# Optimization experiments

Measured on AMD Instinct MI355X. Metric: run time of the kernel, lower is better.

## Reference

```python
import jax, jax.numpy as jnp
import numpy as np

K = 128      # scratch_keys_dim
NP = 3       # n_pointers
P = 200      # program_dim
STEPS = 3    # max_program_steps


def _positional_encoding(max_len=50, d=K):
    pos = np.arange(max_len, dtype=np.float32)[:, None]
    div = np.exp(np.arange(0, d, 2, dtype=np.float32) * (-np.log(10000.0) / d))
    pe = np.zeros((max_len, d), dtype=np.float32)
    pe[:, 0::2] = np.sin(pos * div)
    pe[:, 1::2] = np.cos(pos * div)
    return jnp.asarray(pe)


def setup_inputs() -> dict:
    B, I, L, Vin, Vout = 256, 16, 50, 1000, 512
    H = K * NP
    key = jax.random.key(0)
    ks = jax.random.split(key, 8)
    s = 0.05
    return {
        'instructions': jax.random.randint(ks[0], (I, B), 0, Vin),
        'true_actions': jax.random.randint(ks[1], (L, B), 0, Vout),
        'gate_emb': jax.random.normal(ks[2], (Vin, 2), jnp.float32) * s,
        'program_emb': jax.random.normal(ks[3], (Vin, P), jnp.float32) * s,
        'primitive_emb': jax.random.normal(ks[4], (Vin, Vout), jnp.float32) * s,
        'w_ih': jax.random.normal(ks[5], (3 * H, P), jnp.float32) * s,
        'w_hh': jax.random.normal(ks[6], (3 * H, H), jnp.float32) * s,
        'b_ih': jnp.zeros((3 * H,), jnp.float32),
        'b_hh': jnp.zeros((3 * H,), jnp.float32),
        'scratch_keys': _positional_encoding(),
        'init_value': jnp.zeros((Vout,), jnp.float32).at[0].set(1.0),  # one-hot eos
    }


def _gru_cell(x, h, w_ih, w_hh, b_ih, b_hh):
    # torch.nn.GRUCell math
    gi = x @ w_ih.T + b_ih
    gh = h @ w_hh.T + b_hh
    i_r, i_z, i_n = jnp.split(gi, 3, axis=-1)
    h_r, h_z, h_n = jnp.split(gh, 3, axis=-1)
    r = jax.nn.sigmoid(i_r + h_r)
    z = jax.nn.sigmoid(i_z + h_z)
    n = jnp.tanh(i_n + r * h_n)
    return (1.0 - z) * n + z * h


def reference(instructions, true_actions, gate_emb, program_emb, primitive_emb,
              w_ih, w_hh, b_ih, b_hh, scratch_keys, init_value):
    I, B = instructions.shape
    L = true_actions.shape[0]
    keys = scratch_keys[:L]                                    # [L,K], broadcast over batch
    h0 = jnp.tile(scratch_keys[0], (B, NP))                    # [B,3K] init executor hidden
    v0 = jnp.broadcast_to(init_value, (B, L, init_value.shape[0]))  # [B,L,Vout]

    def outer(carry, word):
        h, vals = carry
        gate = jax.nn.softmax(gate_emb[word], axis=-1)         # [B,2] (softmax gate activation)
        program = program_emb[word]                            # [B,P]
        primitive = primitive_emb[word]                        # [B,Vout]
        for _ in range(STEPS):
            read_ptr = h[:, K:2 * K]                           # [B,K]
            write_ptr = h[:, 2 * K:3 * K]                      # [B,K]
            read_attn = jax.nn.softmax(jnp.einsum('bk,lk->bl', read_ptr, keys), axis=-1)
            read_value = jnp.einsum('bl,blv->bv', read_attn, vals)
            # gate-weighted mix of primitive and read value
            new_value = gate[:, :1] * primitive + gate[:, 1:] * read_value   # [B,Vout]
            write_mask = jax.nn.softmax(jnp.einsum('bk,lk->bl', write_ptr, keys), axis=-1)
            vals = write_mask[:, :, None] * new_value[:, None, :] + (1.0 - write_mask[:, :, None]) * vals
            h = _gru_cell(program, h, w_ih, w_hh, b_ih, b_hh)
        return (h, vals), None

    (h, vals), _ = jax.lax.scan(outer, (h0, v0), instructions)
    actions = jnp.transpose(jax.nn.log_softmax(vals, axis=-1), (0, 2, 1))  # [B,Vout,L]
    return actions, true_actions.T
```

## Files before the change

### kernel.cpp

```cpp
#include <hip/hip_runtime.h>
#include <math.h>

#define KK     128
#define HH     384
#define H3     1152
#define PP     200
#define LL     50
#define VV     512
#define BB     256
#define II     16
#define NSTEPS 3

#define NT     640
#define KPW    132
#define VP2    258

#define GH4G   12
#define GIG    13
#define WQ4H_UI (GH4G * 3 * 384 * 4)
#define WQI_UI  (GIG  * 3 * 384 * 4)

__device__ __forceinline__ int dot4(unsigned a, unsigned b, int c) {
    return __builtin_amdgcn_sdot4((int)a, (int)b, c, false);
}
__device__ __forceinline__ int dot8(unsigned a, unsigned b, int c) {
    return __builtin_amdgcn_sdot8((int)a, (int)b, c, false);
}
__device__ __forceinline__ float rcpf(float x) { return __builtin_amdgcn_rcpf(x); }
__device__ __forceinline__ float sigm(float x) { return rcpf(1.f + __expf(-x)); }
__device__ __forceinline__ float tanh_fast(float x) {
    float xc = fminf(fmaxf(x, -15.f), 15.f);
    float t = __expf(2.f * xc);
    return 1.f - 2.f * rcpf(t + 1.f);
}
__device__ __forceinline__ int q8(float x, float sc) {
    int q = (int)rintf(x * sc);
    return q < -127 ? -127 : (q > 127 ? 127 : q);
}
__device__ __forceinline__ int q4(float x, float sc) {
    int q = (int)rintf(x * sc);
    return q < -7 ? -7 : (q > 7 ? 7 : q);
}

__global__ void wmax_reduce(const float* __restrict__ w_hh,
                            const float* __restrict__ w_ih,
                            const float* __restrict__ prog_emb,
                            unsigned* __restrict__ scales)
{
    int idx = blockIdx.x * 256 + threadIdx.x;
    int stride = gridDim.x * 256;
    float mh = 0.f, mi = 0.f, mp = 0.f;
    for (int i = idx; i < HH * H3; i += stride) mh = fmaxf(mh, fabsf(w_hh[i]));
    for (int i = idx; i < PP * H3; i += stride) mi = fmaxf(mi, fabsf(w_ih[i]));
    for (int i = idx; i < 1000 * PP; i += stride) mp = fmaxf(mp, fabsf(prog_emb[i]));
    #pragma unroll
    for (int mm = 32; mm >= 1; mm >>= 1) {
        mh = fmaxf(mh, __shfl_xor(mh, mm, 64));
        mi = fmaxf(mi, __shfl_xor(mi, mm, 64));
        mp = fmaxf(mp, __shfl_xor(mp, mm, 64));
    }
    if ((threadIdx.x & 63) == 0) {
        atomicMax(scales,     __float_as_uint(mh));
        atomicMax(scales + 1, __float_as_uint(mi));
        atomicMax(scales + 2, __float_as_uint(mp));
    }
}

__global__ void pack_weights(const float* __restrict__ w_hh,
                             const float* __restrict__ w_ih,
                             const unsigned* __restrict__ scales,
                             unsigned* __restrict__ wq)
{
    int idx = blockIdx.x * 256 + threadIdx.x;
    if (idx < WQ4H_UI) {
        const float sc = 7.f * rcpf(fmaxf(__uint_as_float(scales[0]), 1e-20f));
        int u4 = idx >> 2, m = idx & 3;
        int g = u4 / (3 * 384);
        int r = u4 - g * (3 * 384);
        int s = r / 384, t = r - s * 384;
        int j = t + 384 * s, k = 32 * g + 8 * m;
        const float* wr = w_hh + (long)j * HH + k;
        unsigned pw = 0;
        #pragma unroll
        for (int e = 0; e < 8; ++e) pw |= ((unsigned)(q4(wr[e], sc) & 0xF)) << (4 * e);
        wq[idx] = pw;
    } else if (idx < WQ4H_UI + WQI_UI) {
        const float sc = 127.f * rcpf(fmaxf(__uint_as_float(scales[1]), 1e-20f));
        int q = idx - WQ4H_UI;
        int u4 = q >> 2, m = q & 3;
        int g = u4 / (3 * 384);
        int r = u4 - g * (3 * 384);
        int s = r / 384, t = r - s * 384;
        int j = t + 384 * s, k = 16 * g + 4 * m;
        unsigned pw = 0;
        #pragma unroll
        for (int e = 0; e < 4; ++e) {
            float w = (k + e < PP) ? w_ih[(long)j * PP + k + e] : 0.f;
            pw |= ((unsigned)(q8(w, sc) & 255)) << (8 * e);
        }
        wq[WQ4H_UI + u4 * 4 + m] = pw;
    }
}

struct __align__(16) Smem {
    float2 vals[LL * VP2];
    float  keys[LL * KPW];
    float  h[HH]            __attribute__((aligned(16)));
    unsigned hq4[HH / 8]    __attribute__((aligned(16)));
    unsigned progq[56]      __attribute__((aligned(16)));
    float  rl[52], wl[52];
    float  raw[4][52], wmw[4][52];
    float  rowoff[52];
    float  partial[4 * 52];
};

__global__ __launch_bounds__(NT)
void symop_main(const int* __restrict__ instr,
                const float* __restrict__ gate_emb,
                const float* __restrict__ program_emb,
                const float* __restrict__ primitive_emb,
                const uint4* __restrict__ wqhh,
                const uint4* __restrict__ wqih,
                const unsigned* __restrict__ scales,
                const float* __restrict__ b_ih,
                const float* __restrict__ b_hh,
                const float* __restrict__ keys_g,
                const float* __restrict__ init_value,
                float* __restrict__ out)
{
    __shared__ Smem sm;

    const int tid  = threadIdx.x;
    const int lane = tid & 63;
    const int wid  = tid >> 6;
    const int b    = blockIdx.x;

    const float maxH = fmaxf(__uint_as_float(scales[0]), 1e-20f);
    const float maxI = fmaxf(__uint_as_float(scales[1]), 1e-20f);
    const float maxP = fmaxf(__uint_as_float(scales[2]), 1e-20f);
    const float ghs = maxH * (1.f / 49.f);
    const float gis = maxI * maxP * (1.f / 16129.f);
    const float psc = 127.f * rcpf(maxP);

    for (int idx = tid; idx < LL * KK; idx += NT) {
        int l = idx >> 7, k = idx & 127;
        sm.keys[l * KPW + k] = keys_g[idx];
    }
    float hcur = 0.f;
    if (tid < HH) {
        hcur = keys_g[tid & 127];
        sm.h[tid] = hcur;
    }
    if (tid < HH / 8) {
        unsigned pw = 0;
        #pragma unroll
        for (int e = 0; e < 8; ++e) {
            int q = (int)rintf(keys_g[(8 * tid + e) & 127] * 7.f);
            pw |= ((unsigned)(q & 0xF)) << (4 * e);
        }
        sm.hq4[tid] = pw;
    }
    for (int idx = tid; idx < LL * 256; idx += NT) {
        int l = idx >> 8, c = idx & 255;
        sm.vals[l * VP2 + c] = *(const float2*)(init_value + 2 * c);
    }
    if (tid >= 512 && tid < 512 + 52) {
        int qt = tid - 512;
        int w0 = instr[b];
        const float* pg = program_emb + (long)w0 * PP;
        unsigned pw = 0;
        #pragma unroll
        for (int e = 0; e < 4; ++e) {
            int k = 4 * qt + e;
            float v = (k < PP) ? pg[k] : 0.f;
            pw |= ((unsigned)(q8(v, psc) & 255)) << (8 * e);
        }
        sm.progq[qt] = pw;
    }
    __syncthreads();

    float bh0 = 0, bh1 = 0, bh2 = 0, bi0 = 0, bi1 = 0, bi2 = 0;
    if (tid < HH) {
        bh0 = b_hh[tid]; bh1 = b_hh[tid + HH]; bh2 = b_hh[tid + 2 * HH];
        bi0 = b_ih[tid]; bi1 = b_ih[tid + HH]; bi2 = b_ih[tid + 2 * HH];
    }
    float gic0 = 0, gic1 = 0, gic2 = 0;
    int   gn0 = 0, gn1 = 0, gn2 = 0;

    if (tid < HH) {
        int ia0 = 0, ia1 = 0, ia2 = 0;
        const uint4* wp = wqih + tid;
        #pragma unroll 2
        for (int g = 0; g < GIG; ++g) {
            uint4 w0 = wp[(g * 3 + 0) * 384];
            uint4 w1 = wp[(g * 3 + 1) * 384];
            uint4 w2 = wp[(g * 3 + 2) * 384];
            uint4 hp = *(const uint4*)(sm.progq + 4 * g);
            ia0 = dot4(w0.x, hp.x, ia0); ia0 = dot4(w0.y, hp.y, ia0);
            ia0 = dot4(w0.z, hp.z, ia0); ia0 = dot4(w0.w, hp.w, ia0);
            ia1 = dot4(w1.x, hp.x, ia1); ia1 = dot4(w1.y, hp.y, ia1);
            ia1 = dot4(w1.z, hp.z, ia1); ia1 = dot4(w1.w, hp.w, ia1);
            ia2 = dot4(w2.x, hp.x, ia2); ia2 = dot4(w2.y, hp.y, ia2);
            ia2 = dot4(w2.z, hp.z, ia2); ia2 = dot4(w2.w, hp.w, ia2);
        }
        gic0 = bi0 + (float)ia0 * gis;
        gic1 = bi1 + (float)ia1 * gis;
        gic2 = bi2 + (float)ia2 * gis;
    } else if (tid < HH + 2 * LL) {
        int dd = tid - HH;
        int l = (dd < LL) ? dd : dd - LL;
        const float* p  = (dd < LL) ? (sm.h + KK) : (sm.h + 2 * KK);
        const float* kr = sm.keys + l * KPW;
        float acc = 0.f;
        #pragma unroll 8
        for (int k = 0; k < KK; ++k) acc = fmaf(p[k], kr[k], acc);
        if (dd < LL) sm.rl[l] = acc; else sm.wl[l] = acc;
    }
    __syncthreads();

    for (int i = 0; i < II; ++i) {
        const int word = instr[i * BB + b];
        for (int t = 0; t < NSTEPS; ++t) {
            if (tid < HH) {
                int ia0 = 0, ia1 = 0, ia2 = 0;
                const uint4* wp = wqhh + tid;
                #pragma unroll 2
                for (int g = 0; g < GH4G; ++g) {
                    uint4 w0 = wp[(g * 3 + 0) * 384];
                    uint4 w1 = wp[(g * 3 + 1) * 384];
                    uint4 w2 = wp[(g * 3 + 2) * 384];
                    uint4 hp = *(const uint4*)(sm.hq4 + 4 * g);
                    ia0 = dot8(w0.x, hp.x, ia0); ia0 = dot8(w0.y, hp.y, ia0);
                    ia0 = dot8(w0.z, hp.z, ia0); ia0 = dot8(w0.w, hp.w, ia0);
                    ia1 = dot8(w1.x, hp.x, ia1); ia1 = dot8(w1.y, hp.y, ia1);
                    ia1 = dot8(w1.z, hp.z, ia1); ia1 = dot8(w1.w, hp.w, ia1);
                    ia2 = dot8(w2.x, hp.x, ia2); ia2 = dot8(w2.y, hp.y, ia2);
                    ia2 = dot8(w2.z, hp.z, ia2); ia2 = dot8(w2.w, hp.w, ia2);
                }
                const float gh0 = bh0 + (float)ia0 * ghs;
                const float gh1 = bh1 + (float)ia1 * ghs;
                const float gh2 = bh2 + (float)ia2 * ghs;

                if (i + 1 < II) {
                    const uint4* wi = wqih + tid;
                    if (t == 1) {
                        gn0 = 0; gn1 = 0; gn2 = 0;
                        #pragma unroll 2
                        for (int g = 0; g < 7; ++g) {
                            uint4 w0 = wi[(g * 3 + 0) * 384];
                            uint4 w1 = wi[(g * 3 + 1) * 384];
                            uint4 w2 = wi[(g * 3 + 2) * 384];
                            uint4 hp = *(const uint4*)(sm.progq + 4 * g);
                            gn0 = dot4(w0.x, hp.x, gn0); gn0 = dot4(w0.y, hp.y, gn0);
                            gn0 = dot4(w0.z, hp.z, gn0); gn0 = dot4(w0.w, hp.w, gn0);
                            gn1 = dot4(w1.x, hp.x, gn1); gn1 = dot4(w1.y, hp.y, gn1);
                            gn1 = dot4(w1.z, hp.z, gn1); gn1 = dot4(w1.w, hp.w, gn1);
                            gn2 = dot4(w2.x, hp.x, gn2); gn2 = dot4(w2.y, hp.y, gn2);
                            gn2 = dot4(w2.z, hp.z, gn2); gn2 = dot4(w2.w, hp.w, gn2);
                        }
                    } else if (t == 2) {
                        #pragma unroll 2
                        for (int g = 7; g < GIG; ++g) {
                            uint4 w0 = wi[(g * 3 + 0) * 384];
                            uint4 w1 = wi[(g * 3 + 1) * 384];
                            uint4 w2 = wi[(g * 3 + 2) * 384];
                            uint4 hp = *(const uint4*)(sm.progq + 4 * g);
                            gn0 = dot4(w0.x, hp.x, gn0); gn0 = dot4(w0.y, hp.y, gn0);
                            gn0 = dot4(w0.z, hp.z, gn0); gn0 = dot4(w0.w, hp.w, gn0);
                            gn1 = dot4(w1.x, hp.x, gn1); gn1 = dot4(w1.y, hp.y, gn1);
                            gn1 = dot4(w1.z, hp.z, gn1); gn1 = dot4(w1.w, hp.w, gn1);
                            gn2 = dot4(w2.x, hp.x, gn2); gn2 = dot4(w2.y, hp.y, gn2);
                            gn2 = dot4(w2.z, hp.z, gn2); gn2 = dot4(w2.w, hp.w, gn2);
                        }
                    }
                }

                const float r = sigm(gic0 + gh0);
                const float z = sigm(gic1 + gh1);
                const float n = tanh_fast(gic2 + r * gh2);
                const float hn = (1.f - z) * n + z * hcur;
                hcur = hn;
                sm.h[tid] = hn;
                int q = ((int)rintf(hn * 7.f)) & 0xF;
                unsigned u1 = (unsigned)q | ((unsigned)__shfl_down(q, 1, 64) << 4);
                unsigned u2 = u1 | (__shfl_down((int)u1, 2, 64) << 8);
                unsigned u4 = u2 | (__shfl_down((int)u2, 4, 64) << 16);
                if (!(tid & 7)) sm.hq4[tid >> 3] = u4;
                if (t == 2 && i + 1 < II) {
                    gic0 = bi0 + (float)gn0 * gis;
                    gic1 = bi1 + (float)gn1 * gis;
                    gic2 = bi2 + (float)gn2 * gis;
                }
            } else {
                const int w4 = wid - 6;
                float vr = (lane < LL) ? sm.rl[lane] : -1e30f;
                float vw = (lane < LL) ? sm.wl[lane] : -1e30f;
                float mr = vr, mw = vw;
                #pragma unroll
                for (int mm = 32; mm >= 1; mm >>= 1) {
                    mr = fmaxf(mr, __shfl_xor(mr, mm, 64));
                    mw = fmaxf(mw, __shfl_xor(mw, mm, 64));
                }
                float er = (lane < LL) ? __expf(vr - mr) : 0.f;
                float ew = (lane < LL) ? __expf(vw - mw) : 0.f;
                float sr = er, sw = ew;
                #pragma unroll
                for (int mm = 32; mm >= 1; mm >>= 1) {
                    sr += __shfl_xor(sr, mm, 64);
                    sw += __shfl_xor(sw, mm, 64);
                }
                if (lane < LL) {
                    sm.raw[w4][lane] = er * rcpf(sr);
                    sm.wmw[w4][lane] = ew * rcpf(sw);
                }
                const float ge0 = gate_emb[2 * word], ge1 = gate_emb[2 * word + 1];
                const float gmx = fmaxf(ge0, ge1);
                const float e0 = __expf(ge0 - gmx), e1 = __expf(ge1 - gmx);
                const float g0 = e0 * rcpf(e0 + e1), g1 = 1.0f - g0;
                const float* prim = primitive_emb + (long)word * VV;

                const int c = tid - HH;
                float2 pr = *(const float2*)(prim + 2 * c);
                float rv0 = 0.f, rv1 = 0.f;
                #pragma unroll 10
                for (int l = 0; l < LL; ++l) {
                    float2 vv = sm.vals[l * VP2 + c];
                    rv0 = fmaf(sm.raw[w4][l], vv.x, rv0);
                    rv1 = fmaf(sm.raw[w4][l], vv.y, rv1);
                }
                const float nv0 = g0 * pr.x + g1 * rv0;
                const float nv1 = g0 * pr.y + g1 * rv1;
                #pragma unroll 10
                for (int l = 0; l < LL; ++l) {
                    float2 vv = sm.vals[l * VP2 + c];
                    const float w = sm.wmw[w4][l];
                    vv.x = fmaf(w, nv0 - vv.x, vv.x);
                    vv.y = fmaf(w, nv1 - vv.y, vv.y);
                    sm.vals[l * VP2 + c] = vv;
                }
            }
            __syncthreads();

            if (tid < 4 * 2 * LL) {
                const int dot = tid >> 2;
                const int sub = tid & 3;
                const int l   = (dot < LL) ? dot : dot - LL;
                const float* p  = (dot < LL) ? (sm.h + KK) : (sm.h + 2 * KK);
                const float* kr = sm.keys + l * KPW;
                float acc = 0.f;
                #pragma unroll
                for (int kk = 0; kk < KK / 4; ++kk) {
                    int k = sub + 4 * kk;
                    acc = fmaf(p[k], kr[k], acc);
                }
                acc += __shfl_xor(acc, 1, 64);
                acc += __shfl_xor(acc, 2, 64);
                if (sub == 0) {
                    if (dot < LL) sm.rl[l] = acc; else sm.wl[l] = acc;
                }
            } else if (t == 0 && i + 1 < II && tid >= 512 && tid < 512 + 52) {
                int qt = tid - 512;
                int wn = instr[(i + 1) * BB + b];
                const float* pg = program_emb + (long)wn * PP;
                unsigned pw = 0;
                #pragma unroll
                for (int e = 0; e < 4; ++e) {
                    int k = 4 * qt + e;
                    float v = (k < PP) ? pg[k] : 0.f;
                    pw |= ((unsigned)(q8(v, psc) & 255)) << (8 * e);
                }
                sm.progq[qt] = pw;
            }
            __syncthreads();
        }
    }

    if (tid < 256) {
        #pragma unroll 5
        for (int l = 0; l < LL; ++l) {
            float2 vv = sm.vals[l * VP2 + tid];
            float e = __expf(vv.x) + __expf(vv.y);
            #pragma unroll
            for (int mm = 32; mm >= 1; mm >>= 1) e += __shfl_xor(e, mm, 64);
            if (lane == 0) sm.partial[wid * 52 + l] = e;
        }
    }
    __syncthreads();
    if (tid < LL) {
        float s = 0.f;
        #pragma unroll
        for (int w = 0; w < 4; ++w) s += sm.partial[w * 52 + tid];
        sm.rowoff[tid] = logf(s);
    }
    __syncthreads();

    if (tid < 256) {
        float* ob0 = out + (long)b * VV * LL + (long)(2 * tid) * LL;
        float* ob1 = ob0 + LL;
        #pragma unroll 5
        for (int l = 0; l < LL; l += 2) {
            float2 va = sm.vals[l * VP2 + tid];
            float2 vb = sm.vals[(l + 1) * VP2 + tid];
            float o0 = sm.rowoff[l], o1 = sm.rowoff[l + 1];
            *(float2*)(ob0 + l) = make_float2(va.x - o0, vb.x - o1);
            *(float2*)(ob1 + l) = make_float2(va.y - o0, vb.y - o1);
        }
    }
}

__global__ void ta_copy(const int* __restrict__ ta, float* __restrict__ out2)
{
    int idx = blockIdx.x * 256 + threadIdx.x;
    if (idx < BB * LL) {
        int b2 = idx / LL, l = idx % LL;
        out2[idx] = (float)ta[l * BB + b2];
    }
}

extern "C" void kernel_launch(void* const* d_in, const int* in_sizes, int n_in,
                              void* d_out, int out_size, void* d_ws, size_t ws_size,
                              hipStream_t stream)
{
    const int*   instr        = (const int*)  d_in[0];
    const int*   true_actions = (const int*)  d_in[1];
    const float* gate_emb     = (const float*)d_in[2];
    const float* program_emb  = (const float*)d_in[3];
    const float* primitive_emb= (const float*)d_in[4];
    const float* w_ih         = (const float*)d_in[5];
    const float* w_hh         = (const float*)d_in[6];
    const float* b_ih         = (const float*)d_in[7];
    const float* b_hh         = (const float*)d_in[8];
    const float* scratch_keys = (const float*)d_in[9];
    const float* init_value   = (const float*)d_in[10];

    unsigned* scales = (unsigned*)d_ws;
    unsigned* wq     = (unsigned*)d_ws + 4;
    const uint4* wqhh = (const uint4*)wq;
    const uint4* wqih = (const uint4*)(wq + WQ4H_UI);

    hipMemsetAsync(scales, 0, 12, stream);
    wmax_reduce<<<256, 256, 0, stream>>>(w_hh, w_ih, program_emb, scales);
    {
        int total = WQ4H_UI + WQI_UI;
        pack_weights<<<(total + 255) / 256, 256, 0, stream>>>(w_hh, w_ih, scales, wq);
    }

    float* out = (float*)d_out;
    float* out_actions = out;
    float* out_ta      = out + (long)BB * VV * LL;

    symop_main<<<BB, NT, 0, stream>>>(instr, gate_emb, program_emb, primitive_emb,
                                      wqhh, wqih, scales, b_ih, b_hh,
                                      scratch_keys, init_value, out_actions);

    ta_copy<<<(BB * LL + 255) / 256, 256, 0, stream>>>(true_actions, out_ta);
}
```

Baseline: 310.6 us.

## Fuse pointer-key logits into value waves with int8 dot4 and double-buffered hidden

Removes the separate fp32 phase that computed read/write attention logits, and the second barrier per step that followed it. The value-update waves now compute the logits themselves using int8-quantized keys and an int8 copy of the hidden state with sdot4. The quantized hidden state is double-buffered (hq4/hq8 indexed by parity), so the GRU threads can write the next state while the other waves read the current one, leaving one barrier per step. Attention logits now carry int8 quantization error, and each GRU step does extra shuffle/pack work to produce both 4-bit and 8-bit copies of h.

New measurement: 302.7 us (median of 2 runs). 2.6% less time.

```diff
diff --git a/kernel.cpp b/kernel.cpp
--- a/kernel.cpp
+++ b/kernel.cpp
@@ -12,8 +12,8 @@
 #define NSTEPS 3
 
 #define NT     640
-#define KPW    132
 #define VP2    258
+#define KQP    33
 
 #define GH4G   12
 #define GIG    13
@@ -104,11 +104,10 @@
 
 struct __align__(16) Smem {
     float2 vals[LL * VP2];
-    float  keys[LL * KPW];
-    float  h[HH]            __attribute__((aligned(16)));
-    unsigned hq4[HH / 8]    __attribute__((aligned(16)));
+    unsigned keysq[LL * KQP + 16] __attribute__((aligned(16)));
+    unsigned hq4[2][48]     __attribute__((aligned(16)));
+    unsigned hq8[2][96]     __attribute__((aligned(16)));
     unsigned progq[56]      __attribute__((aligned(16)));
-    float  rl[52], wl[52];
     float  raw[4][52], wmw[4][52];
     float  rowoff[52];
     float  partial[4 * 52];
@@ -141,24 +140,35 @@
     const float ghs = maxH * (1.f / 49.f);
     const float gis = maxI * maxP * (1.f / 16129.f);
     const float psc = 127.f * rcpf(maxP);
-
-    for (int idx = tid; idx < LL * KK; idx += NT) {
-        int l = idx >> 7, k = idx & 127;
-        sm.keys[l * KPW + k] = keys_g[idx];
-    }
+    const float lsc = 1.f / 16129.f;
+
     float hcur = 0.f;
-    if (tid < HH) {
-        hcur = keys_g[tid & 127];
-        sm.h[tid] = hcur;
-    }
-    if (tid < HH / 8) {
+    if (tid < HH) hcur = keys_g[tid & 127];
+    for (int idx = tid; idx < LL * 32; idx += NT) {
+        int l = idx >> 5, kk = idx & 31;
+        const float* kr = keys_g + l * KK + 4 * kk;
+        unsigned pw = 0;
+        #pragma unroll
+        for (int e = 0; e < 4; ++e) pw |= ((unsigned)(q8(kr[e], 127.f) & 255)) << (8 * e);
+        sm.keysq[l * KQP + kk] = pw;
+    }
+    if (tid < 96) {
+        unsigned pw = 0;
+        #pragma unroll
+        for (int e = 0; e < 4; ++e) {
+            int q = q8(keys_g[(4 * tid + e) & 127], 127.f);
+            pw |= ((unsigned)(q & 255)) << (8 * e);
+        }
+        sm.hq8[0][tid] = pw;
+    } else if (tid >= 128 && tid < 128 + 48) {
+        int u = tid - 128;
         unsigned pw = 0;
         #pragma unroll
         for (int e = 0; e < 8; ++e) {
-            int q = (int)rintf(keys_g[(8 * tid + e) & 127] * 7.f);
+            int q = q4(keys_g[(8 * u + e) & 127], 7.f);
             pw |= ((unsigned)(q & 0xF)) << (4 * e);
         }
-        sm.hq4[tid] = pw;
+        sm.hq4[0][u] = pw;
     }
     for (int idx = tid; idx < LL * 256; idx += NT) {
         int l = idx >> 8, c = idx & 255;
@@ -206,18 +216,9 @@
         gic0 = bi0 + (float)ia0 * gis;
         gic1 = bi1 + (float)ia1 * gis;
         gic2 = bi2 + (float)ia2 * gis;
-    } else if (tid < HH + 2 * LL) {
-        int dd = tid - HH;
-        int l = (dd < LL) ? dd : dd - LL;
-        const float* p  = (dd < LL) ? (sm.h + KK) : (sm.h + 2 * KK);
-        const float* kr = sm.keys + l * KPW;
-        float acc = 0.f;
-        #pragma unroll 8
-        for (int k = 0; k < KK; ++k) acc = fmaf(p[k], kr[k], acc);
-        if (dd < LL) sm.rl[l] = acc; else sm.wl[l] = acc;
-    }
-    __syncthreads();
-
+    }
+
+    int par = 0;
     for (int i = 0; i < II; ++i) {
         const int word = instr[i * BB + b];
         for (int t = 0; t < NSTEPS; ++t) {
@@ -229,7 +230,7 @@
                     uint4 w0 = wp[(g * 3 + 0) * 384];
                     uint4 w1 = wp[(g * 3 + 1) * 384];
                     uint4 w2 = wp[(g * 3 + 2) * 384];
-                    uint4 hp = *(const uint4*)(sm.hq4 + 4 * g);
+                    uint4 hp = *(const uint4*)(sm.hq4[par] + 4 * g);
                     ia0 = dot8(w0.x, hp.x, ia0); ia0 = dot8(w0.y, hp.y, ia0);
                     ia0 = dot8(w0.z, hp.z, ia0); ia0 = dot8(w0.w, hp.w, ia0);
                     ia1 = dot8(w1.x, hp.x, ia1); ia1 = dot8(w1.y, hp.y, ia1);
@@ -280,12 +281,16 @@
                 const float n = tanh_fast(gic2 + r * gh2);
                 const float hn = (1.f - z) * n + z * hcur;
                 hcur = hn;
-                sm.h[tid] = hn;
-                int q = ((int)rintf(hn * 7.f)) & 0xF;
-                unsigned u1 = (unsigned)q | ((unsigned)__shfl_down(q, 1, 64) << 4);
-                unsigned u2 = u1 | (__shfl_down((int)u1, 2, 64) << 8);
-                unsigned u4 = u2 | (__shfl_down((int)u2, 4, 64) << 16);
-                if (!(tid & 7)) sm.hq4[tid >> 3] = u4;
+                int q8v = ((int)rintf(hn * 127.f)) & 255;
+                unsigned v1 = (unsigned)q8v | ((unsigned)(__shfl_down(q8v, 1, 64) & 255) << 8);
+                unsigned v2 = v1 | ((unsigned)__shfl_down((int)v1, 2, 64) << 16);
+                if (!(tid & 3)) sm.hq8[par ^ 1][tid >> 2] = v2;
+                int q4v = ((int)rintf(hn * 7.f)) & 0xF;
+                unsigned u1 = (unsigned)q4v | ((unsigned)(__shfl_down(q4v, 1, 64) & 0xF) << 4);
+                unsigned u2 = u1 | ((unsigned)(__shfl_down((int)u1, 2, 64) & 0xFF) << 8);
+                unsigned u4 = u2 | ((unsigned)__shfl_down((int)u2, 4, 64) << 16);
+                if (!(tid & 7)) sm.hq4[par ^ 1][tid >> 3] = u4;
+
                 if (t == 2 && i + 1 < II) {
                     gic0 = bi0 + (float)gn0 * gis;
                     gic1 = bi1 + (float)gn1 * gis;
@@ -293,16 +298,33 @@
                 }
             } else {
                 const int w4 = wid - 6;
-                float vr = (lane < LL) ? sm.rl[lane] : -1e30f;
-                float vw = (lane < LL) ? sm.wl[lane] : -1e30f;
-                float mr = vr, mw = vw;
+                float rlog = -1e30f, wlog = -1e30f;
+                if (lane < LL) {
+                    int ir = 0, iw = 0;
+                    const unsigned* kq = sm.keysq + lane * KQP;
+                    const uint4* h8r = (const uint4*)(sm.hq8[par] + 32);
+                    const uint4* h8w = (const uint4*)(sm.hq8[par] + 64);
+                    #pragma unroll
+                    for (int o = 0; o < 8; ++o) {
+                        uint4 hr = h8r[o], hw = h8w[o];
+                        unsigned k0 = kq[4 * o], k1 = kq[4 * o + 1];
+                        unsigned k2 = kq[4 * o + 2], k3 = kq[4 * o + 3];
+                        ir = dot4(k0, hr.x, ir); ir = dot4(k1, hr.y, ir);
+                        ir = dot4(k2, hr.z, ir); ir = dot4(k3, hr.w, ir);
+                        iw = dot4(k0, hw.x, iw); iw = dot4(k1, hw.y, iw);
+                        iw = dot4(k2, hw.z, iw); iw = dot4(k3, hw.w, iw);
+                    }
+                    rlog = (float)ir * lsc;
+                    wlog = (float)iw * lsc;
+                }
+                float mr = rlog, mw = wlog;
                 #pragma unroll
                 for (int mm = 32; mm >= 1; mm >>= 1) {
                     mr = fmaxf(mr, __shfl_xor(mr, mm, 64));
                     mw = fmaxf(mw, __shfl_xor(mw, mm, 64));
                 }
-                float er = (lane < LL) ? __expf(vr - mr) : 0.f;
-                float ew = (lane < LL) ? __expf(vw - mw) : 0.f;
+                float er = (lane < LL) ? __expf(rlog - mr) : 0.f;
+                float ew = (lane < LL) ? __expf(wlog - mw) : 0.f;
                 float sr = er, sw = ew;
                 #pragma unroll
                 for (int mm = 32; mm >= 1; mm >>= 1) {
@@ -338,40 +360,22 @@
                     vv.y = fmaf(w, nv1 - vv.y, vv.y);
                     sm.vals[l * VP2 + c] = vv;
                 }
+                if (t == 0 && i + 1 < II && tid >= 512 && tid < 512 + 52) {
+                    int qt = tid - 512;
+                    int wn = instr[(i + 1) * BB + b];
+                    const float* pg = program_emb + (long)wn * PP;
+                    unsigned pw = 0;
+                    #pragma unroll
+                    for (int e = 0; e < 4; ++e) {
+                        int k = 4 * qt + e;
+                        float v = (k < PP) ? pg[k] : 0.f;
+                        pw |= ((unsigned)(q8(v, psc) & 255)) << (8 * e);
+                    }
+                    sm.progq[qt] = pw;
+                }
             }
             __syncthreads();
-
-            if (tid < 4 * 2 * LL) {
-                const int dot = tid >> 2;
-                const int sub = tid & 3;
-                const int l   = (dot < LL) ? dot : dot - LL;
-                const float* p  = (dot < LL) ? (sm.h + KK) : (sm.h + 2 * KK);
-                const float* kr = sm.keys + l * KPW;
-                float acc = 0.f;
-                #pragma unroll
-                for (int kk = 0; kk < KK / 4; ++kk) {
-                    int k = sub + 4 * kk;
-                    acc = fmaf(p[k], kr[k], acc);
-                }
-                acc += __shfl_xor(acc, 1, 64);
-                acc += __shfl_xor(acc, 2, 64);
-                if (sub == 0) {
-                    if (dot < LL) sm.rl[l] = acc; else sm.wl[l] = acc;
-                }
-            } else if (t == 0 && i + 1 < II && tid >= 512 && tid < 512 + 52) {
-                int qt = tid - 512;
-                int wn = instr[(i + 1) * BB + b];
-                const float* pg = program_emb + (long)wn * PP;
-                unsigned pw = 0;
-                #pragma unroll
-                for (int e = 0; e < 4; ++e) {
-                    int k = 4 * qt + e;
-                    float v = (k < PP) ? pg[k] : 0.f;
-                    pw |= ((unsigned)(q8(v, psc) & 255)) << (8 * e);
-                }
-                sm.progq[qt] = pw;
-            }
-            __syncthreads();
+            par ^= 1;
         }
     }
 
```
